# Performance work log

Hardware: AMD Instinct MI355X
Metric: run time of the kernel (lower is better)

## Reference

```python
import jax, jax.numpy as jnp
import numpy as np

ALPHA = 1.0  # Student-t degrees of freedom (module default)


def setup_inputs() -> dict:
    key = jax.random.key(0)
    k1, k2 = jax.random.split(key)
    N, D, K = 65536, 512, 256
    x = jax.random.normal(k1, (N, D), dtype=jnp.float32)
    clusters = jax.random.normal(k2, (K, D), dtype=jnp.float32)
    return {"x": x, "clusters": clusters}


def reference(x, clusters):
    # Squared Euclidean distance via norm expansion + GEMM (same math as
    # sum((x[:,None,:] - clusters[None,:,:])**2, axis=2); original then takes
    # sqrt and immediately re-squares, so we use sqdist directly).
    x_sq = jnp.sum(x * x, axis=1, keepdims=True)            # [N,1]
    c_sq = jnp.sum(clusters * clusters, axis=1)             # [K]
    sqdist = x_sq + c_sq[None, :] - 2.0 * (x @ clusters.T)  # [N,K]
    sqdist = jnp.maximum(sqdist, 0.0)
    # Student's t kernel: q_ij = (1 + d^2/alpha)^(-(alpha+1)/2)
    q = (1.0 + sqdist / ALPHA) ** (-(ALPHA + 1.0) / 2.0)
    # Row-normalize to soft assignments
    return q / jnp.sum(q, axis=1, keepdims=True)
```

## Files before the change

kernel.cpp:

```cpp
#include <hip/hip_runtime.h>
#include <stdint.h>

typedef unsigned short u16;
typedef __attribute__((ext_vector_type(8))) short short8_t;
typedef __attribute__((ext_vector_type(4))) float f32x4;

#define D_DIM 512
#define K_CL  256
#define BM    128
#define BK    64
#define NSTEP (D_DIM / BK)

__device__ __forceinline__ u16 f2bf(float f) {
  union { float f; uint32_t u; } v; v.f = f;
  uint32_t r = v.u + 0x7fffu + ((v.u >> 16) & 1u);
  return (u16)(r >> 16);
}

__device__ __forceinline__ short8_t pack8(float4 f0, float4 f1) {
  union { u16 u[8]; short8_t v; } pk;
  pk.u[0] = f2bf(f0.x); pk.u[1] = f2bf(f0.y);
  pk.u[2] = f2bf(f0.z); pk.u[3] = f2bf(f0.w);
  pk.u[4] = f2bf(f1.x); pk.u[5] = f2bf(f1.y);
  pk.u[6] = f2bf(f1.z); pk.u[7] = f2bf(f1.w);
  return pk.v;
}

__global__ void prep_kernel(const float* __restrict__ clusters,
                            u16* __restrict__ cb, float* __restrict__ csq) {
  int k = blockIdx.x;
  int t = threadIdx.x;
  float4 f = ((const float4*)(clusters + (size_t)k * D_DIM))[t];
  ushort4 u;
  u.x = f2bf(f.x); u.y = f2bf(f.y); u.z = f2bf(f.z); u.w = f2bf(f.w);
  ((ushort4*)(cb + (size_t)k * D_DIM))[t] = u;
  float s = f.x*f.x + f.y*f.y + f.z*f.z + f.w*f.w;
  #pragma unroll
  for (int m = 1; m < 64; m <<= 1) s += __shfl_xor(s, m, 64);
  __shared__ float part[2];
  if ((t & 63) == 0) part[t >> 6] = s;
  __syncthreads();
  if (t == 0) csq[k] = part[0] + part[1];
}

__global__ __launch_bounds__(512, 4)
void cluster_kernel(const float* __restrict__ x,
                    const u16* __restrict__ cb,
                    const float* __restrict__ csq,
                    float* __restrict__ out) {
  __shared__ u16 lB[2 * K_CL * BK];

  const int tid  = threadIdx.x;
  const int lane = tid & 63;
  const int w    = tid >> 6;
  const int l16  = lane & 15;
  const int quad = lane >> 4;
  const int row0 = blockIdx.x * BM;

  const int arow = row0 + w * 16 + l16;
  const float4* xg = (const float4*)(x + (size_t)arow * D_DIM + quad * 8);

  const int o0   = tid * 16;
  const int n0   = o0 >> 7;
  const int skb0 = (o0 & 127) ^ ((n0 & 7) << 4);
  const int o1   = 8192 + tid * 16;
  const int n1   = o1 >> 7;
  const int skb1 = (o1 & 127) ^ ((n1 & 7) << 4);
  const u16* sp0 = cb + (size_t)n0 * D_DIM + (skb0 >> 1);
  const u16* sp1 = cb + (size_t)n1 * D_DIM + (skb1 >> 1);

  const int c3 = (l16 & 3) << 4;
  const int h  = (l16 & 4) << 4;
  const int p  = l16 * 128 + ((quad * 16) ^ c3);
  const int p0 = p + h;
  const int p1 = p + (h ^ 64);

  f32x4 acc[16];
  #pragma unroll
  for (int i = 0; i < 16; ++i) acc[i] = (f32x4){0.f, 0.f, 0.f, 0.f};

  {
    char* dstb = (char*)lB + tid * 16;
    __builtin_amdgcn_global_load_lds((const __attribute__((address_space(1))) void*)sp0,
        (__attribute__((address_space(3))) void*)(dstb),          16, 0, 0);
    __builtin_amdgcn_global_load_lds((const __attribute__((address_space(1))) void*)sp1,
        (__attribute__((address_space(3))) void*)(dstb + 8192),   16, 0, 0);
    __builtin_amdgcn_global_load_lds((const __attribute__((address_space(1))) void*)(sp0 + 65536),
        (__attribute__((address_space(3))) void*)(dstb + 16384),  16, 0, 0);
    __builtin_amdgcn_global_load_lds((const __attribute__((address_space(1))) void*)(sp1 + 65536),
        (__attribute__((address_space(3))) void*)(dstb + 24576),  16, 0, 0);
  }
  float4 a0 = xg[0], a1 = xg[1], a2 = xg[8], a3 = xg[9];

  float sq = 0.f;

  for (int step = 0; step < NSTEP; ++step) {
    __syncthreads();

    sq += a0.x*a0.x + a0.y*a0.y + a0.z*a0.z + a0.w*a0.w
        + a1.x*a1.x + a1.y*a1.y + a1.z*a1.z + a1.w*a1.w
        + a2.x*a2.x + a2.y*a2.y + a2.z*a2.z + a2.w*a2.w
        + a3.x*a3.x + a3.y*a3.y + a3.z*a3.z + a3.w*a3.w;
    short8_t aF0 = pack8(a0, a1);
    short8_t aF1 = pack8(a2, a3);

    if (step + 1 < NSTEP) {
      xg += 16;
      a0 = xg[0]; a1 = xg[1]; a2 = xg[8]; a3 = xg[9];
      sp0 += BK; sp1 += BK;
      char* dstb = (char*)lB + (((step + 1) & 1) << 15) + tid * 16;
      __builtin_amdgcn_global_load_lds((const __attribute__((address_space(1))) void*)sp0,
          (__attribute__((address_space(3))) void*)(dstb),          16, 0, 0);
      __builtin_amdgcn_global_load_lds((const __attribute__((address_space(1))) void*)sp1,
          (__attribute__((address_space(3))) void*)(dstb + 8192),   16, 0, 0);
      __builtin_amdgcn_global_load_lds((const __attribute__((address_space(1))) void*)(sp0 + 65536),
          (__attribute__((address_space(3))) void*)(dstb + 16384),  16, 0, 0);
      __builtin_amdgcn_global_load_lds((const __attribute__((address_space(1))) void*)(sp1 + 65536),
          (__attribute__((address_space(3))) void*)(dstb + 24576),  16, 0, 0);
    }

    const char* pb = (const char*)lB + ((step & 1) << 15);
    const short8_t* q0 = (const short8_t*)(pb + p0);
    const short8_t* q1 = (const short8_t*)(pb + p1);
    #pragma unroll
    for (int ni = 0; ni < 16; ++ni) {
      short8_t b0 = q0[ni * 128];
      short8_t b1 = q1[ni * 128];
      acc[ni] = __builtin_amdgcn_mfma_f32_16x16x32_bf16(aF0, b0, acc[ni], 0, 0, 0);
      acc[ni] = __builtin_amdgcn_mfma_f32_16x16x32_bf16(aF1, b1, acc[ni], 0, 0, 0);
    }
  }

  sq += __shfl_xor(sq, 16, 64);
  sq += __shfl_xor(sq, 32, 64);
  float xs[4];
  #pragma unroll
  for (int v = 0; v < 4; ++v)
    xs[v] = __shfl(sq, quad * 4 + v, 64);

  float cs[16];
  #pragma unroll
  for (int ni = 0; ni < 16; ++ni) cs[ni] = csq[ni * 16 + l16];

  float rs[4] = {0.f, 0.f, 0.f, 0.f};
  #pragma unroll
  for (int ni = 0; ni < 16; ++ni) {
    #pragma unroll
    for (int v = 0; v < 4; ++v) {
      float d = xs[v] + cs[ni] - 2.0f * acc[ni][v];
      d = fmaxf(d, 0.f);
      float qv = __builtin_amdgcn_rcpf(1.0f + d);
      acc[ni][v] = qv;
      rs[v] += qv;
    }
  }
  #pragma unroll
  for (int v = 0; v < 4; ++v) {
    rs[v] += __shfl_xor(rs[v], 1, 64);
    rs[v] += __shfl_xor(rs[v], 2, 64);
    rs[v] += __shfl_xor(rs[v], 4, 64);
    rs[v] += __shfl_xor(rs[v], 8, 64);
    rs[v] = __builtin_amdgcn_rcpf(rs[v]);
  }
  #pragma unroll
  for (int v = 0; v < 4; ++v) {
    float* orow = out + (size_t)(row0 + w * 16 + quad * 4 + v) * K_CL;
    #pragma unroll
    for (int ni = 0; ni < 16; ++ni)
      orow[ni * 16 + l16] = acc[ni][v] * rs[v];
  }
}

extern "C" void kernel_launch(void* const* d_in, const int* in_sizes, int n_in,
                              void* d_out, int out_size, void* d_ws, size_t ws_size,
                              hipStream_t stream) {
  const float* x        = (const float*)d_in[0];
  const float* clusters = (const float*)d_in[1];
  float* out = (float*)d_out;
  const int N = in_sizes[0] / D_DIM;

  u16*   cb  = (u16*)d_ws;
  float* csq = (float*)((char*)d_ws + (size_t)K_CL * D_DIM * sizeof(u16));

  prep_kernel<<<K_CL, 128, 0, stream>>>(clusters, cb, csq);
  cluster_kernel<<<N / BM, 512, 0, stream>>>(x, cb, csq, out);
}
```

Measured before the change: 219.4 us.

## Read cluster bf16 fragments directly from global memory, drop LDS staging

```diff
diff --git a/kernel.cpp b/kernel.cpp
--- a/kernel.cpp
+++ b/kernel.cpp
@@ -48,8 +48,6 @@
                     const u16* __restrict__ cb,
                     const float* __restrict__ csq,
                     float* __restrict__ out) {
-  __shared__ u16 lB[2 * K_CL * BK];
-
   const int tid  = threadIdx.x;
   const int lane = tid & 63;
   const int w    = tid >> 6;
@@ -60,43 +58,16 @@
   const int arow = row0 + w * 16 + l16;
   const float4* xg = (const float4*)(x + (size_t)arow * D_DIM + quad * 8);
 
-  const int o0   = tid * 16;
-  const int n0   = o0 >> 7;
-  const int skb0 = (o0 & 127) ^ ((n0 & 7) << 4);
-  const int o1   = 8192 + tid * 16;
-  const int n1   = o1 >> 7;
-  const int skb1 = (o1 & 127) ^ ((n1 & 7) << 4);
-  const u16* sp0 = cb + (size_t)n0 * D_DIM + (skb0 >> 1);
-  const u16* sp1 = cb + (size_t)n1 * D_DIM + (skb1 >> 1);
-
-  const int c3 = (l16 & 3) << 4;
-  const int h  = (l16 & 4) << 4;
-  const int p  = l16 * 128 + ((quad * 16) ^ c3);
-  const int p0 = p + h;
-  const int p1 = p + (h ^ 64);
+  const char* bbase = (const char*)cb + l16 * 1024 + quad * 16;
 
   f32x4 acc[16];
   #pragma unroll
   for (int i = 0; i < 16; ++i) acc[i] = (f32x4){0.f, 0.f, 0.f, 0.f};
 
-  {
-    char* dstb = (char*)lB + tid * 16;
-    __builtin_amdgcn_global_load_lds((const __attribute__((address_space(1))) void*)sp0,
-        (__attribute__((address_space(3))) void*)(dstb),          16, 0, 0);
-    __builtin_amdgcn_global_load_lds((const __attribute__((address_space(1))) void*)sp1,
-        (__attribute__((address_space(3))) void*)(dstb + 8192),   16, 0, 0);
-    __builtin_amdgcn_global_load_lds((const __attribute__((address_space(1))) void*)(sp0 + 65536),
-        (__attribute__((address_space(3))) void*)(dstb + 16384),  16, 0, 0);
-    __builtin_amdgcn_global_load_lds((const __attribute__((address_space(1))) void*)(sp1 + 65536),
-        (__attribute__((address_space(3))) void*)(dstb + 24576),  16, 0, 0);
-  }
   float4 a0 = xg[0], a1 = xg[1], a2 = xg[8], a3 = xg[9];
-
   float sq = 0.f;
 
   for (int step = 0; step < NSTEP; ++step) {
-    __syncthreads();
-
     sq += a0.x*a0.x + a0.y*a0.y + a0.z*a0.z + a0.w*a0.w
         + a1.x*a1.x + a1.y*a1.y + a1.z*a1.z + a1.w*a1.w
         + a2.x*a2.x + a2.y*a2.y + a2.z*a2.z + a2.w*a2.w
@@ -107,25 +78,13 @@
     if (step + 1 < NSTEP) {
       xg += 16;
       a0 = xg[0]; a1 = xg[1]; a2 = xg[8]; a3 = xg[9];
-      sp0 += BK; sp1 += BK;
-      char* dstb = (char*)lB + (((step + 1) & 1) << 15) + tid * 16;
-      __builtin_amdgcn_global_load_lds((const __attribute__((address_space(1))) void*)sp0,
-          (__attribute__((address_space(3))) void*)(dstb),          16, 0, 0);
-      __builtin_amdgcn_global_load_lds((const __attribute__((address_space(1))) void*)sp1,
-          (__attribute__((address_space(3))) void*)(dstb + 8192),   16, 0, 0);
-      __builtin_amdgcn_global_load_lds((const __attribute__((address_space(1))) void*)(sp0 + 65536),
-          (__attribute__((address_space(3))) void*)(dstb + 16384),  16, 0, 0);
-      __builtin_amdgcn_global_load_lds((const __attribute__((address_space(1))) void*)(sp1 + 65536),
-          (__attribute__((address_space(3))) void*)(dstb + 24576),  16, 0, 0);
     }
 
-    const char* pb = (const char*)lB + ((step & 1) << 15);
-    const short8_t* q0 = (const short8_t*)(pb + p0);
-    const short8_t* q1 = (const short8_t*)(pb + p1);
+    const char* bp = bbase + step * 128;
     #pragma unroll
     for (int ni = 0; ni < 16; ++ni) {
-      short8_t b0 = q0[ni * 128];
-      short8_t b1 = q1[ni * 128];
+      short8_t b0 = *(const short8_t*)(bp + ni * 16384);
+      short8_t b1 = *(const short8_t*)(bp + ni * 16384 + 64);
       acc[ni] = __builtin_amdgcn_mfma_f32_16x16x32_bf16(aF0, b0, acc[ni], 0, 0, 0);
       acc[ni] = __builtin_amdgcn_mfma_f32_16x16x32_bf16(aF1, b1, acc[ni], 0, 0, 0);
     }
```

New measurement: 305.0 us. 39.0% more time.

## Replace per-step syncthreads with partial vmcnt wait and barrier, unroll K loop

Applied to the files above, without the earlier changes.

```diff
diff --git a/kernel.cpp b/kernel.cpp
--- a/kernel.cpp
+++ b/kernel.cpp
@@ -1,4 +1,5 @@
 #include <hip/hip_runtime.h>
+#include <hip/hip_bf16.h>
 #include <stdint.h>
 
 typedef unsigned short u16;
@@ -9,7 +10,7 @@
 #define K_CL  256
 #define BM    128
 #define BK    64
-#define NSTEP (D_DIM / BK)
+#define NSTEP 8
 
 __device__ __forceinline__ u16 f2bf(float f) {
   union { float f; uint32_t u; } v; v.f = f;
@@ -17,12 +18,12 @@
   return (u16)(r >> 16);
 }
 
-__device__ __forceinline__ short8_t pack8(float4 f0, float4 f1) {
-  union { u16 u[8]; short8_t v; } pk;
-  pk.u[0] = f2bf(f0.x); pk.u[1] = f2bf(f0.y);
-  pk.u[2] = f2bf(f0.z); pk.u[3] = f2bf(f0.w);
-  pk.u[4] = f2bf(f1.x); pk.u[5] = f2bf(f1.y);
-  pk.u[6] = f2bf(f1.z); pk.u[7] = f2bf(f1.w);
+__device__ __forceinline__ short8_t pack8(const float4& f0, const float4& f1) {
+  union { __hip_bfloat16 h[8]; short8_t v; } pk;
+  pk.h[0] = __float2bfloat16(f0.x); pk.h[1] = __float2bfloat16(f0.y);
+  pk.h[2] = __float2bfloat16(f0.z); pk.h[3] = __float2bfloat16(f0.w);
+  pk.h[4] = __float2bfloat16(f1.x); pk.h[5] = __float2bfloat16(f1.y);
+  pk.h[6] = __float2bfloat16(f1.z); pk.h[7] = __float2bfloat16(f1.w);
   return pk.v;
 }
 
@@ -48,7 +49,7 @@
                     const u16* __restrict__ cb,
                     const float* __restrict__ csq,
                     float* __restrict__ out) {
-  __shared__ u16 lB[2 * K_CL * BK];
+  __shared__ __align__(128) u16 lB[2 * K_CL * BK];
 
   const int tid  = threadIdx.x;
   const int lane = tid & 63;
@@ -57,8 +58,7 @@
   const int quad = lane >> 4;
   const int row0 = blockIdx.x * BM;
 
-  const int arow = row0 + w * 16 + l16;
-  const float4* xg = (const float4*)(x + (size_t)arow * D_DIM + quad * 8);
+  const float4* xg = (const float4*)(x + (size_t)(row0 + w * 16 + l16) * D_DIM + quad * 8);
 
   const int o0   = tid * 16;
   const int n0   = o0 >> 7;
@@ -78,6 +78,8 @@
   f32x4 acc[16];
   #pragma unroll
   for (int i = 0; i < 16; ++i) acc[i] = (f32x4){0.f, 0.f, 0.f, 0.f};
+
+  float4 a0, a1, a2, a3;
 
   {
     char* dstb = (char*)lB + tid * 16;
@@ -90,12 +92,29 @@
     __builtin_amdgcn_global_load_lds((const __attribute__((address_space(1))) void*)(sp1 + 65536),
         (__attribute__((address_space(3))) void*)(dstb + 24576),  16, 0, 0);
   }
-  float4 a0 = xg[0], a1 = xg[1], a2 = xg[8], a3 = xg[9];
+  a0 = xg[0]; a1 = xg[1]; a2 = xg[8]; a3 = xg[9];
+  asm volatile("s_waitcnt vmcnt(4)" ::: "memory");
+  __builtin_amdgcn_s_barrier();
+  __builtin_amdgcn_sched_barrier(0);
 
   float sq = 0.f;
 
+  #pragma unroll
   for (int step = 0; step < NSTEP; ++step) {
-    __syncthreads();
+
+    if (step + 1 < NSTEP) {
+      const u16* q0 = sp0 + (step + 1) * BK;
+      const u16* q1 = sp1 + (step + 1) * BK;
+      char* dstb = (char*)lB + (((step + 1) & 1) << 15) + tid * 16;
+      __builtin_amdgcn_global_load_lds((const __attribute__((address_space(1))) void*)q0,
+          (__attribute__((address_space(3))) void*)(dstb),          16, 0, 0);
+      __builtin_amdgcn_global_load_lds((const __attribute__((address_space(1))) void*)q1,
+          (__attribute__((address_space(3))) void*)(dstb + 8192),   16, 0, 0);
+      __builtin_amdgcn_global_load_lds((const __attribute__((address_space(1))) void*)(q0 + 65536),
+          (__attribute__((address_space(3))) void*)(dstb + 16384),  16, 0, 0);
+      __builtin_amdgcn_global_load_lds((const __attribute__((address_space(1))) void*)(q1 + 65536),
+          (__attribute__((address_space(3))) void*)(dstb + 24576),  16, 0, 0);
+    }
 
     sq += a0.x*a0.x + a0.y*a0.y + a0.z*a0.z + a0.w*a0.w
         + a1.x*a1.x + a1.y*a1.y + a1.z*a1.z + a1.w*a1.w
@@ -105,29 +124,23 @@
     short8_t aF1 = pack8(a2, a3);
 
     if (step + 1 < NSTEP) {
-      xg += 16;
-      a0 = xg[0]; a1 = xg[1]; a2 = xg[8]; a3 = xg[9];
-      sp0 += BK; sp1 += BK;
-      char* dstb = (char*)lB + (((step + 1) & 1) << 15) + tid * 16;
-      __builtin_amdgcn_global_load_lds((const __attribute__((address_space(1))) void*)sp0,
-          (__attribute__((address_space(3))) void*)(dstb),          16, 0, 0);
-      __builtin_amdgcn_global_load_lds((const __attribute__((address_space(1))) void*)sp1,
-          (__attribute__((address_space(3))) void*)(dstb + 8192),   16, 0, 0);
-      __builtin_amdgcn_global_load_lds((const __attribute__((address_space(1))) void*)(sp0 + 65536),
-          (__attribute__((address_space(3))) void*)(dstb + 16384),  16, 0, 0);
-      __builtin_amdgcn_global_load_lds((const __attribute__((address_space(1))) void*)(sp1 + 65536),
-          (__attribute__((address_space(3))) void*)(dstb + 24576),  16, 0, 0);
+      const float4* g = xg + (step + 1) * 16;
+      a0 = g[0]; a1 = g[1]; a2 = g[8]; a3 = g[9];
     }
 
     const char* pb = (const char*)lB + ((step & 1) << 15);
-    const short8_t* q0 = (const short8_t*)(pb + p0);
-    const short8_t* q1 = (const short8_t*)(pb + p1);
     #pragma unroll
     for (int ni = 0; ni < 16; ++ni) {
-      short8_t b0 = q0[ni * 128];
-      short8_t b1 = q1[ni * 128];
+      short8_t b0 = *(const short8_t*)(pb + ni * 2048 + p0);
+      short8_t b1 = *(const short8_t*)(pb + ni * 2048 + p1);
       acc[ni] = __builtin_amdgcn_mfma_f32_16x16x32_bf16(aF0, b0, acc[ni], 0, 0, 0);
       acc[ni] = __builtin_amdgcn_mfma_f32_16x16x32_bf16(aF1, b1, acc[ni], 0, 0, 0);
+    }
+
+    if (step + 1 < NSTEP) {
+      asm volatile("s_waitcnt vmcnt(4)" ::: "memory");
+      __builtin_amdgcn_s_barrier();
+      __builtin_amdgcn_sched_barrier(0);
     }
   }
 
```

Result: slower. 302.4 us (+37.8%).
